# Kernel tuning notes

Hardware: AMD Instinct MI355X
Metric: run time of the kernel (lower is better)

## Reference

```python
import jax, jax.numpy as jnp
import numpy as np

D_IN = 1024
D_OUT = 1024
NUM_HEAD = 16
HEAD_DIM = D_OUT // NUM_HEAD
CTX = 2048


def setup_inputs() -> dict:
    key = jax.random.key(0)
    ks = jax.random.split(key, 7)
    s = 0.02
    x = jax.random.normal(ks[0], (2, CTX, D_IN), dtype=jnp.float32)
    Wq = jax.random.normal(ks[1], (D_IN, D_OUT), dtype=jnp.float32) * s
    Wk = jax.random.normal(ks[2], (D_IN, D_OUT), dtype=jnp.float32) * s
    Wv = jax.random.normal(ks[3], (D_IN, D_OUT), dtype=jnp.float32) * s
    Wo = jax.random.normal(ks[4], (D_OUT, D_OUT), dtype=jnp.float32) * s
    bo = jax.random.normal(ks[5], (D_OUT,), dtype=jnp.float32) * s
    return {"x": x, "Wq": Wq, "Wk": Wk, "Wv": Wv, "Wo": Wo, "bo": bo}


def reference(x, Wq, Wk, Wv, Wo, bo):
    B, T, _ = x.shape
    # QKV projections, split into heads: [B, H, T, hd]
    def split_heads(y):
        return y.reshape(B, T, NUM_HEAD, HEAD_DIM).transpose(0, 2, 1, 3)
    q = split_heads(x @ Wq)
    k = split_heads(x @ Wk)
    v = split_heads(x @ Wv)
    # scaled causal attention scores [B, H, T, T]
    scores = jnp.einsum("bhqd,bhkd->bhqk", q, k) / jnp.sqrt(
        jnp.asarray(HEAD_DIM, dtype=x.dtype))
    causal = jnp.tril(jnp.ones((T, T), dtype=bool))  # mask buffer triu(diag=1) -> keep lower tri
    scores = jnp.where(causal[None, None], scores, jnp.asarray(-jnp.inf, dtype=x.dtype))
    attn = jax.nn.softmax(scores, axis=-1)
    # dropout with droprate=0.0 is identity
    ctx = jnp.einsum("bhqk,bhkd->bhqd", attn, v)
    ctx = ctx.transpose(0, 2, 1, 3).reshape(B, T, D_OUT)
    return ctx @ Wo + bo
```

## Files before the change

### kernel.cpp

```cpp
#include <hip/hip_runtime.h>

typedef __bf16 bf16x8 __attribute__((ext_vector_type(8)));
typedef float f32x4 __attribute__((ext_vector_type(4)));
typedef float f32x16 __attribute__((ext_vector_type(16)));
typedef unsigned int u32x4 __attribute__((ext_vector_type(4)));

__device__ inline unsigned short f2bf(float f) {
    unsigned int x = __builtin_bit_cast(unsigned int, f);
    x += 0x7fff + ((x >> 16) & 1);
    return (unsigned short)(x >> 16);
}

__device__ __forceinline__ void gl_lds16(const unsigned short* g, unsigned short* l)
{
    __builtin_amdgcn_global_load_lds(
        (const __attribute__((address_space(1))) void*)g,
        (__attribute__((address_space(3))) void*)l, 16, 0, 0);
}

__global__ __launch_bounds__(256)
void prep(const float* __restrict__ x, unsigned short* __restrict__ xb,
          const float* __restrict__ Wq, const float* __restrict__ Wk,
          const float* __restrict__ Wv, unsigned short* __restrict__ wT)
{
    __shared__ unsigned short T[64][72];
    if (blockIdx.x < 2048) {
        const size_t i = ((size_t)blockIdx.x * 256 + threadIdx.x) * 8;
        float4 a = *reinterpret_cast<const float4*>(x + i);
        float4 b = *reinterpret_cast<const float4*>(x + i + 4);
        unsigned short t[8] = { f2bf(a.x), f2bf(a.y), f2bf(a.z), f2bf(a.w),
                                f2bf(b.x), f2bf(b.y), f2bf(b.z), f2bf(b.w) };
        *reinterpret_cast<uint4*>(xb + i) = *reinterpret_cast<uint4*>(t);
        return;
    }
    const int blk = blockIdx.x - 2048;
    const int z = blk >> 8, within = blk & 255;
    const float* W = (z == 0) ? Wq : (z == 1) ? Wk : Wv;
    unsigned short* dstBase = wT + (size_t)z * 1024 * 1024;
    const int k0 = (within >> 4) * 64, n0 = (within & 15) * 64;
    const int r = threadIdx.x >> 2, c0 = (threadIdx.x & 3) * 16;
    const float* src = W + (size_t)(k0 + r) * 1024 + n0 + c0;
    #pragma unroll
    for (int j = 0; j < 16; j += 4) {
        float4 f = *reinterpret_cast<const float4*>(src + j);
        T[r][c0 + j]     = f2bf(f.x);
        T[r][c0 + j + 1] = f2bf(f.y);
        T[r][c0 + j + 2] = f2bf(f.z);
        T[r][c0 + j + 3] = f2bf(f.w);
    }
    __syncthreads();
    unsigned short* dst = dstBase + (size_t)(n0 + r) * 1024 + k0 + c0;
    #pragma unroll
    for (int h = 0; h < 2; ++h) {
        unsigned short t8[8];
        #pragma unroll
        for (int j = 0; j < 8; ++j) t8[j] = T[c0 + h * 8 + j][r];
        *reinterpret_cast<uint4*>(dst + h * 8) = *reinterpret_cast<uint4*>(t8);
    }
}

__global__ __launch_bounds__(256)
void wconv(const float* __restrict__ W, unsigned short* __restrict__ wT)
{
    __shared__ unsigned short T[64][72];
    const int k0 = blockIdx.y * 64, n0 = blockIdx.x * 64;
    const int r = threadIdx.x >> 2, c0 = (threadIdx.x & 3) * 16;
    const float* src = W + (size_t)(k0 + r) * 1024 + n0 + c0;
    #pragma unroll
    for (int j = 0; j < 16; j += 4) {
        float4 f = *reinterpret_cast<const float4*>(src + j);
        T[r][c0 + j]     = f2bf(f.x);
        T[r][c0 + j + 1] = f2bf(f.y);
        T[r][c0 + j + 2] = f2bf(f.z);
        T[r][c0 + j + 3] = f2bf(f.w);
    }
    __syncthreads();
    unsigned short* dst = wT + (size_t)(n0 + r) * 1024 + k0 + c0;
    #pragma unroll
    for (int h = 0; h < 2; ++h) {
        unsigned short t8[8];
        #pragma unroll
        for (int j = 0; j < 8; ++j) t8[j] = T[c0 + h * 8 + j][r];
        *reinterpret_cast<uint4*>(dst + h * 8) = *reinterpret_cast<uint4*>(t8);
    }
}

__global__ __launch_bounds__(512, 4)
void gemm8p(const unsigned short* __restrict__ A,
            const unsigned short* __restrict__ BT,
            unsigned short* __restrict__ qb,
            unsigned short* __restrict__ kb,
            unsigned short* __restrict__ vT)
{
    __shared__ unsigned short As[2][128 * 64];
    __shared__ unsigned short Bs[2][192 * 64];

    const int tid  = threadIdx.x;
    const int wave = tid >> 6, lane = tid & 63;
    const int quad = lane >> 4, l16 = lane & 15;
    const int wm = wave >> 2, wn = wave & 3;
    const int mBase = blockIdx.y * 128, nBase = blockIdx.x * 192;

    f32x4 acc[4][3] = {};

    const int arow = tid >> 3;
    const int u8   = (tid & 7) ^ (arow & 7);
    const int rx   = l16 & 7;

    auto stage = [&](int kb0, int buf) {
        #pragma unroll
        for (int i = 0; i < 2; ++i)
            gl_lds16(A + (size_t)(mBase + i * 64 + arow) * 1024 + kb0 + u8 * 8,
                     &As[buf][(i * 512 + wave * 64) * 8]);
        #pragma unroll
        for (int i = 0; i < 3; ++i)
            gl_lds16(BT + (size_t)(nBase + i * 64 + arow) * 1024 + kb0 + u8 * 8,
                     &Bs[buf][(i * 512 + wave * 64) * 8]);
    };

    stage(0, 0);
    __syncthreads();

    for (int t = 0; t < 16; ++t) {
        const int buf = t & 1;
        if (t + 1 < 16)
            stage((t + 1) * 64, buf ^ 1);

        #pragma unroll
        for (int kh = 0; kh < 2; ++kh) {
            bf16x8 af[4], bf[3];
            #pragma unroll
            for (int mr = 0; mr < 4; ++mr) {
                const int row = wm * 64 + mr * 16 + l16;
                af[mr] = *reinterpret_cast<const bf16x8*>(
                    &As[buf][row * 64 + (((kh * 4 + quad) ^ rx) * 8)]);
            }
            #pragma unroll
            for (int nr = 0; nr < 3; ++nr) {
                const int row = wn * 48 + nr * 16 + l16;
                bf[nr] = *reinterpret_cast<const bf16x8*>(
                    &Bs[buf][row * 64 + (((kh * 4 + quad) ^ rx) * 8)]);
            }
            #pragma unroll
            for (int mr = 0; mr < 4; ++mr)
                #pragma unroll
                for (int nr = 0; nr < 3; ++nr)
                    acc[mr][nr] = __builtin_amdgcn_mfma_f32_16x16x32_bf16(
                        af[mr], bf[nr], acc[mr][nr], 0, 0, 0);
        }

        if (t + 1 < 16) {
            asm volatile("s_waitcnt vmcnt(0)" ::: "memory");
            __builtin_amdgcn_s_barrier();
        }
    }

    #pragma unroll
    for (int mr = 0; mr < 4; ++mr) {
        const int row0 = mBase + wm * 64 + mr * 16 + quad * 4;
        #pragma unroll
        for (int nr = 0; nr < 3; ++nr) {
            const int col = nBase + wn * 48 + nr * 16 + l16;
            if (col < 1024) {
                #pragma unroll
                for (int i = 0; i < 4; ++i)
                    qb[(size_t)(row0 + i) * 1024 + col] = f2bf(acc[mr][nr][i]);
            } else if (col < 2048) {
                #pragma unroll
                for (int i = 0; i < 4; ++i)
                    kb[(size_t)(row0 + i) * 1024 + col - 1024] = f2bf(acc[mr][nr][i]);
            } else {
                unsigned short t4[4] = { f2bf(acc[mr][nr][0]), f2bf(acc[mr][nr][1]),
                                         f2bf(acc[mr][nr][2]), f2bf(acc[mr][nr][3]) };
                *reinterpret_cast<uint2*>(&vT[(size_t)(col - 2048) * 4096 + row0]) =
                    *reinterpret_cast<uint2*>(t4);
            }
        }
    }
}

__global__ __launch_bounds__(256)
void gemm128o(const unsigned short* __restrict__ A,
              const unsigned short* __restrict__ BT,
              float* __restrict__ out, const float* __restrict__ bias)
{
    __shared__ unsigned short As[128 * 32];
    __shared__ unsigned short Bs[128 * 32];

    const int tid = threadIdx.x;
    const int wave = tid >> 6, lane = tid & 63, quad = lane >> 4, l16 = lane & 15;
    const int wm = wave >> 1, wn = wave & 1;
    const int mBase = blockIdx.y * 128, nBase = blockIdx.x * 128;

    f32x4 acc[4][4] = {};

    const int srow = lane >> 2, sko = (lane & 3) * 8;

    for (int kb = 0; kb < 1024; kb += 32) {
        __syncthreads();
        #pragma unroll
        for (int j = 0; j < 2; ++j) {
            const int seg = wave * 2 + j;
            gl_lds16(A  + (size_t)(mBase + seg * 16 + srow) * 1024 + kb + sko,
                     As + seg * 512);
            gl_lds16(BT + (size_t)(nBase + seg * 16 + srow) * 1024 + kb + sko,
                     Bs + seg * 512);
        }
        __syncthreads();

        bf16x8 af[4], bf[4];
        #pragma unroll
        for (int t = 0; t < 4; ++t) {
            af[t] = *reinterpret_cast<const bf16x8*>(&As[(wm * 64 + t * 16 + l16) * 32 + quad * 8]);
            bf[t] = *reinterpret_cast<const bf16x8*>(&Bs[(wn * 64 + t * 16 + l16) * 32 + quad * 8]);
        }
        #pragma unroll
        for (int ti = 0; ti < 4; ++ti)
            #pragma unroll
            for (int tj = 0; tj < 4; ++tj)
                acc[ti][tj] = __builtin_amdgcn_mfma_f32_16x16x32_bf16(
                    af[ti], bf[tj], acc[ti][tj], 0, 0, 0);
    }

    #pragma unroll
    for (int ti = 0; ti < 4; ++ti) {
        const int row0 = mBase + wm * 64 + ti * 16 + quad * 4;
        #pragma unroll
        for (int tj = 0; tj < 4; ++tj) {
            const int col = nBase + wn * 64 + tj * 16 + l16;
            const float ba = bias[col];
            #pragma unroll
            for (int i = 0; i < 4; ++i)
                out[(size_t)(row0 + i) * 1024 + col] = acc[ti][tj][i] + ba;
        }
    }
}

__global__ __launch_bounds__(256, 2)
void attn12(const unsigned short* __restrict__ q,
            const unsigned short* __restrict__ k,
            const unsigned short* __restrict__ vT,
            unsigned short* __restrict__ ctx)
{
    __shared__ unsigned short Ks[3][64 * 64];
    __shared__ unsigned short Vs[3][64 * 64];
    __shared__ float Lt[8 * 64];

    const int tid  = threadIdx.x;
    const int wave = tid >> 6, lane = tid & 63;
    const int q32 = lane & 31, hi = lane >> 5;
    const int slice = wave & 1;
    const int ks    = wave >> 1;
    const int L   = (int)(blockIdx.x + (blockIdx.y << 4));
    const int xcd = L & 7, idx = L >> 3;
    const int bh  = xcd * 4 + (idx >> 4);
    const int j   = idx & 15;
    const int b = bh >> 4, h = bh & 15;
    const int tokBase = b * 2048;
    const int colBase = h * 64;
    const int qtA = 31 - j, qtB = j;
    const int qloA = qtA * 64 + slice * 32;
    const int qloB = qtB * 64 + slice * 32;

    bf16x8 aqA[4], aqB[4];
    {
        const unsigned short* ra = q + (size_t)(tokBase + qloA + q32) * 1024 + colBase + hi * 8;
        const unsigned short* rb = q + (size_t)(tokBase + qloB + q32) * 1024 + colBase + hi * 8;
        #pragma unroll
        for (int c = 0; c < 4; ++c) {
            aqA[c] = *reinterpret_cast<const bf16x8*>(ra + c * 16);
            aqB[c] = *reinterpret_cast<const bf16x8*>(rb + c * 16);
        }
    }
    #pragma unroll
    for (int c = 0; c < 4; ++c)
        asm volatile("" :: "v"(aqA[c]), "v"(aqB[c]));

    f32x16 oA[2] = {}, oB[2] = {};
    float lsA = 0.0f, lsB = 0.0f;

    const int s0 = (wave * 2 + 0) * 64 + lane;
    const int s1 = (wave * 2 + 1) * 64 + lane;
    const int r0 = s0 >> 3, sw0 = (s0 & 7) ^ (r0 & 7);
    const int r1 = s1 >> 3, sw1 = (s1 & 7) ^ (r1 & 7);
    const size_t kOff0 = (size_t)r0 * 1024 + colBase + sw0 * 8;
    const size_t kOff1 = (size_t)r1 * 1024 + colBase + sw1 * 8;
    const size_t vOff0 = (size_t)(colBase + r0) * 4096 + sw0 * 8;
    const size_t vOff1 = (size_t)(colBase + r1) * 4096 + sw1 * 8;

    auto stage = [&](int tok0, int buf) {
        gl_lds16(k  + (size_t)tok0 * 1024 + kOff0, &Ks[buf][(wave * 2 + 0) * 512]);
        gl_lds16(k  + (size_t)tok0 * 1024 + kOff1, &Ks[buf][(wave * 2 + 1) * 512]);
        gl_lds16(vT + vOff0 + tok0,                &Vs[buf][(wave * 2 + 0) * 512]);
        gl_lds16(vT + vOff1 + tok0,                &Vs[buf][(wave * 2 + 1) * 512]);
    };

    bf16x8 ak[4];
    bf16x8 bv[2][2];

    const int nkt = qtA + 1;
    stage(tokBase, 0);
    stage(tokBase + 64, 1);

    int cur = 0;
    const int krowK = ks * 32 + q32;
    for (int kt = 0; kt < nkt; ++kt) {
        if (kt + 1 < nkt) asm volatile("s_waitcnt vmcnt(4)" ::: "memory");
        else              asm volatile("s_waitcnt vmcnt(0)" ::: "memory");
        __builtin_amdgcn_s_barrier();
        asm volatile("" ::: "memory");

        const int stg = (cur == 0) ? 2 : cur - 1;
        if (kt + 2 < nkt)
            stage(tokBase + (kt + 2) * 64, stg);

        const unsigned short* KsB = Ks[cur];
        const unsigned short* VsB = Vs[cur];
        #pragma unroll
        for (int c = 0; c < 4; ++c) {
            const int u = c * 2 + hi;
            ak[c] = *reinterpret_cast<const bf16x8*>(
                &KsB[krowK * 64 + ((u ^ (krowK & 7)) * 8)]);
        }
        #pragma unroll
        for (int kc = 0; kc < 2; ++kc)
            #pragma unroll
            for (int dh = 0; dh < 2; ++dh) {
                const int vrow = dh * 32 + q32;
                const int u = ks * 4 + kc * 2 + hi;
                bv[kc][dh] = *reinterpret_cast<const bf16x8*>(
                    &VsB[vrow * 64 + ((u ^ (vrow & 7)) * 8)]);
            }

        const int klo = kt * 64 + ks * 32;
        const bool dB = (klo <= qloB + 31);
        const bool dA = (klo <= qloA + 31);

        if (dB) {
            f32x16 scA = (f32x16)0.0f, scB = (f32x16)0.0f;
            #pragma unroll
            for (int c = 0; c < 4; ++c) {
                scA = __builtin_amdgcn_mfma_f32_32x32x16_bf16(ak[c], aqA[c], scA, 0, 0, 0);
                scB = __builtin_amdgcn_mfma_f32_32x32x16_bf16(ak[c], aqB[c], scB, 0, 0, 0);
            }
            float pA[16], pB[16];
            #pragma unroll
            for (int r = 0; r < 16; ++r) {
                pA[r] = __expf(scA[r] * 0.125f);
                pB[r] = __expf(scB[r] * 0.125f);
            }
            if (klo + 31 > qloB) {
                #pragma unroll
                for (int r = 0; r < 16; ++r) {
                    const int krow = (r & 3) + 8 * (r >> 2) + 4 * hi;
                    if (klo + krow > qloB + q32) pB[r] = 0.0f;
                }
            }
            #pragma unroll
            for (int r = 0; r < 16; ++r) { lsA += pA[r]; lsB += pB[r]; }
            unsigned int pkA[8], pkB[8];
            #pragma unroll
            for (int i = 0; i < 8; ++i) {
                asm("v_cvt_pk_bf16_f32 %0, %1, %2"
                    : "=v"(pkA[i]) : "v"(pA[2 * i]), "v"(pA[2 * i + 1]));
                asm("v_cvt_pk_bf16_f32 %0, %1, %2"
                    : "=v"(pkB[i]) : "v"(pB[2 * i]), "v"(pB[2 * i + 1]));
            }
            #pragma unroll
            for (int kc = 0; kc < 2; ++kc) {
                unsigned int xa0 = pkA[kc * 4 + 0], ya0 = pkA[kc * 4 + 2];
                unsigned int xa1 = pkA[kc * 4 + 1], ya1 = pkA[kc * 4 + 3];
                unsigned int xb0 = pkB[kc * 4 + 0], yb0 = pkB[kc * 4 + 2];
                unsigned int xb1 = pkB[kc * 4 + 1], yb1 = pkB[kc * 4 + 3];
                asm("v_permlane32_swap_b32 %0, %1" : "+v"(xa0), "+v"(ya0));
                asm("v_permlane32_swap_b32 %0, %1" : "+v"(xa1), "+v"(ya1));
                asm("v_permlane32_swap_b32 %0, %1" : "+v"(xb0), "+v"(yb0));
                asm("v_permlane32_swap_b32 %0, %1" : "+v"(xb1), "+v"(yb1));
                const u32x4 wa = { xa0, xa1, ya0, ya1 };
                const u32x4 wb = { xb0, xb1, yb0, yb1 };
                const bf16x8 paA = __builtin_bit_cast(bf16x8, wa);
                const bf16x8 paB = __builtin_bit_cast(bf16x8, wb);
                #pragma unroll
                for (int dh = 0; dh < 2; ++dh) {
                    oA[dh] = __builtin_amdgcn_mfma_f32_32x32x16_bf16(paA, bv[kc][dh], oA[dh], 0, 0, 0);
                    oB[dh] = __builtin_amdgcn_mfma_f32_32x32x16_bf16(paB, bv[kc][dh], oB[dh], 0, 0, 0);
                }
            }
        } else if (dA) {
            f32x16 sc = (f32x16)0.0f;
            #pragma unroll
            for (int c = 0; c < 4; ++c)
                sc = __builtin_amdgcn_mfma_f32_32x32x16_bf16(ak[c], aqA[c], sc, 0, 0, 0);
            float p[16];
            #pragma unroll
            for (int r = 0; r < 16; ++r) p[r] = __expf(sc[r] * 0.125f);
            if (klo + 31 > qloA) {
                #pragma unroll
                for (int r = 0; r < 16; ++r) {
                    const int krow = (r & 3) + 8 * (r >> 2) + 4 * hi;
                    if (klo + krow > qloA + q32) p[r] = 0.0f;
                }
            }
            #pragma unroll
            for (int r = 0; r < 16; ++r) lsA += p[r];
            unsigned int pk[8];
            #pragma unroll
            for (int i = 0; i < 8; ++i)
                asm("v_cvt_pk_bf16_f32 %0, %1, %2"
                    : "=v"(pk[i]) : "v"(p[2 * i]), "v"(p[2 * i + 1]));
            #pragma unroll
            for (int kc = 0; kc < 2; ++kc) {
                unsigned int x0 = pk[kc * 4 + 0], y0 = pk[kc * 4 + 2];
                unsigned int x1 = pk[kc * 4 + 1], y1 = pk[kc * 4 + 3];
                asm("v_permlane32_swap_b32 %0, %1" : "+v"(x0), "+v"(y0));
                asm("v_permlane32_swap_b32 %0, %1" : "+v"(x1), "+v"(y1));
                const u32x4 wv = { x0, x1, y0, y1 };
                const bf16x8 pa = __builtin_bit_cast(bf16x8, wv);
                #pragma unroll
                for (int dh = 0; dh < 2; ++dh)
                    oA[dh] = __builtin_amdgcn_mfma_f32_32x32x16_bf16(pa, bv[kc][dh], oA[dh], 0, 0, 0);
            }
        }
        cur = (cur == 2) ? 0 : cur + 1;
    }

    float* Obuf = reinterpret_cast<float*>(&Ks[0][0]);

    __syncthreads();
    Lt[(wave * 2 + 0) * 64 + lane] = lsA;
    Lt[(wave * 2 + 1) * 64 + lane] = lsB;

    auto writePartial = [&](const f32x16 (&o)[2]) {
        float* slot = Obuf + slice * 2048;
        #pragma unroll
        for (int r = 0; r < 16; ++r) {
            const int row = (r & 3) + 8 * (r >> 2) + 4 * hi;
            #pragma unroll
            for (int dh = 0; dh < 2; ++dh)
                slot[row * 64 + dh * 32 + q32] = o[dh][r];
        }
    };
    auto finalize = [&](int t, int qt, const f32x16 (&o)[2]) {
        const float lf = Lt[(slice * 2 + t) * 64 + q32]
                       + Lt[(slice * 2 + t) * 64 + 32 + q32]
                       + Lt[((slice + 2) * 2 + t) * 64 + q32]
                       + Lt[((slice + 2) * 2 + t) * 64 + 32 + q32];
        const float inv = 1.0f / lf;
        const float* slot = Obuf + slice * 2048;
        #pragma unroll
        for (int r = 0; r < 16; ++r) {
            const int row = (r & 3) + 8 * (r >> 2) + 4 * hi;
            const float invr = __shfl(inv, row);
            const size_t gr = (size_t)(tokBase + qt * 64 + slice * 32 + row) * 1024 + colBase;
            #pragma unroll
            for (int dh = 0; dh < 2; ++dh)
                ctx[gr + dh * 32 + q32] =
                    f2bf((o[dh][r] + slot[row * 64 + dh * 32 + q32]) * invr);
        }
    };

    if (ks == 1) writePartial(oA);
    __syncthreads();
    if (ks == 0) finalize(0, qtA, oA);
    __syncthreads();
    if (ks == 0) writePartial(oB);
    __syncthreads();
    if (ks == 1) finalize(1, qtB, oB);
}

extern "C" void kernel_launch(void* const* d_in, const int* in_sizes, int n_in,
                              void* d_out, int out_size, void* d_ws, size_t ws_size,
                              hipStream_t stream)
{
    const float* x  = (const float*)d_in[0];
    const float* Wq = (const float*)d_in[1];
    const float* Wk = (const float*)d_in[2];
    const float* Wv = (const float*)d_in[3];
    const float* Wo = (const float*)d_in[4];
    const float* bo = (const float*)d_in[5];
    float* out = (float*)d_out;

    unsigned short* xb     = (unsigned short*)d_ws;
    unsigned short* qb     = xb + (size_t)4096 * 1024;
    unsigned short* kb     = qb + (size_t)4096 * 1024;
    unsigned short* vT     = kb + (size_t)4096 * 1024;
    unsigned short* ctx    = xb;
    unsigned short* wqkvT  = (unsigned short*)d_out;
    unsigned short* woT    = kb;

    prep<<<2816, 256, 0, stream>>>(x, xb, Wq, Wk, Wv, wqkvT);

    gemm8p<<<dim3(16, 32), 512, 0, stream>>>(xb, wqkvT, qb, kb, vT);

    attn12<<<dim3(16, 32), 256, 0, stream>>>(qb, kb, vT, ctx);

    wconv<<<dim3(16, 16), 256, 0, stream>>>(Wo, woT);

    gemm128o<<<dim3(8, 32), 256, 0, stream>>>(ctx, woT, out, bo);
}
```

Measured before the change: 175.8 us.

## Rewrite output projection GEMM with double-buffered swizzled LDS and 128x64 tiles

Replaces the output-projection GEMM with a version that double-buffers LDS tiles so the next K-slab load overlaps with MFMA work, uses a larger K step of 64, and XOR-swizzles LDS layout to avoid bank conflicts. The tile shrinks to 128x64 so the grid grows from 256 to 512 blocks, which is meant to fill more CUs, with launch bounds allowing two blocks per CU. This costs more LDS per block and a larger share of redundant A loads.

```diff
diff --git a/kernel.cpp b/kernel.cpp
--- a/kernel.cpp
+++ b/kernel.cpp
@@ -179,59 +179,84 @@
     }
 }
 
-__global__ __launch_bounds__(256)
-void gemm128o(const unsigned short* __restrict__ A,
-              const unsigned short* __restrict__ BT,
-              float* __restrict__ out, const float* __restrict__ bias)
-{
-    __shared__ unsigned short As[128 * 32];
-    __shared__ unsigned short Bs[128 * 32];
-
-    const int tid = threadIdx.x;
-    const int wave = tid >> 6, lane = tid & 63, quad = lane >> 4, l16 = lane & 15;
+__global__ __launch_bounds__(256, 2)
+void gemm_op(const unsigned short* __restrict__ A,
+             const unsigned short* __restrict__ BT,
+             float* __restrict__ out, const float* __restrict__ bias)
+{
+    __shared__ unsigned short As[2][128 * 64];
+    __shared__ unsigned short Bs[2][64 * 64];
+
+    const int tid  = threadIdx.x;
+    const int wave = tid >> 6, lane = tid & 63;
+    const int quad = lane >> 4, l16 = lane & 15;
     const int wm = wave >> 1, wn = wave & 1;
-    const int mBase = blockIdx.y * 128, nBase = blockIdx.x * 128;
-
-    f32x4 acc[4][4] = {};
-
-    const int srow = lane >> 2, sko = (lane & 3) * 8;
-
-    for (int kb = 0; kb < 1024; kb += 32) {
-        __syncthreads();
-        #pragma unroll
-        for (int j = 0; j < 2; ++j) {
-            const int seg = wave * 2 + j;
-            gl_lds16(A  + (size_t)(mBase + seg * 16 + srow) * 1024 + kb + sko,
-                     As + seg * 512);
-            gl_lds16(BT + (size_t)(nBase + seg * 16 + srow) * 1024 + kb + sko,
-                     Bs + seg * 512);
-        }
-        __syncthreads();
-
-        bf16x8 af[4], bf[4];
-        #pragma unroll
-        for (int t = 0; t < 4; ++t) {
-            af[t] = *reinterpret_cast<const bf16x8*>(&As[(wm * 64 + t * 16 + l16) * 32 + quad * 8]);
-            bf[t] = *reinterpret_cast<const bf16x8*>(&Bs[(wn * 64 + t * 16 + l16) * 32 + quad * 8]);
-        }
-        #pragma unroll
-        for (int ti = 0; ti < 4; ++ti)
-            #pragma unroll
-            for (int tj = 0; tj < 4; ++tj)
-                acc[ti][tj] = __builtin_amdgcn_mfma_f32_16x16x32_bf16(
-                    af[ti], bf[tj], acc[ti][tj], 0, 0, 0);
-    }
-
-    #pragma unroll
-    for (int ti = 0; ti < 4; ++ti) {
-        const int row0 = mBase + wm * 64 + ti * 16 + quad * 4;
-        #pragma unroll
-        for (int tj = 0; tj < 4; ++tj) {
-            const int col = nBase + wn * 64 + tj * 16 + l16;
+    const int mBase = blockIdx.y * 128, nBase = blockIdx.x * 64;
+
+    f32x4 acc[4][2] = {};
+
+    const int arow = tid >> 3;
+    const int u8   = (tid & 7) ^ (arow & 7);
+    const int rx   = l16 & 7;
+
+    auto stage = [&](int kb0, int buf) {
+        #pragma unroll
+        for (int i = 0; i < 4; ++i)
+            gl_lds16(A + (size_t)(mBase + i * 32 + arow) * 1024 + kb0 + u8 * 8,
+                     &As[buf][(i * 256 + tid) * 8]);
+        #pragma unroll
+        for (int i = 0; i < 2; ++i)
+            gl_lds16(BT + (size_t)(nBase + i * 32 + arow) * 1024 + kb0 + u8 * 8,
+                     &Bs[buf][(i * 256 + tid) * 8]);
+    };
+
+    stage(0, 0);
+    __syncthreads();
+
+    for (int t = 0; t < 16; ++t) {
+        const int buf = t & 1;
+        if (t + 1 < 16)
+            stage((t + 1) * 64, buf ^ 1);
+
+        #pragma unroll
+        for (int kh = 0; kh < 2; ++kh) {
+            bf16x8 af[4], bf[2];
+            #pragma unroll
+            for (int mr = 0; mr < 4; ++mr) {
+                const int row = wm * 64 + mr * 16 + l16;
+                af[mr] = *reinterpret_cast<const bf16x8*>(
+                    &As[buf][row * 64 + (((kh * 4 + quad) ^ rx) * 8)]);
+            }
+            #pragma unroll
+            for (int nr = 0; nr < 2; ++nr) {
+                const int row = wn * 32 + nr * 16 + l16;
+                bf[nr] = *reinterpret_cast<const bf16x8*>(
+                    &Bs[buf][row * 64 + (((kh * 4 + quad) ^ rx) * 8)]);
+            }
+            #pragma unroll
+            for (int mr = 0; mr < 4; ++mr)
+                #pragma unroll
+                for (int nr = 0; nr < 2; ++nr)
+                    acc[mr][nr] = __builtin_amdgcn_mfma_f32_16x16x32_bf16(
+                        af[mr], bf[nr], acc[mr][nr], 0, 0, 0);
+        }
+
+        if (t + 1 < 16) {
+            asm volatile("s_waitcnt vmcnt(0)" ::: "memory");
+            __builtin_amdgcn_s_barrier();
+        }
+    }
+
+    #pragma unroll
+    for (int mr = 0; mr < 4; ++mr) {
+        const int row0 = mBase + wm * 64 + mr * 16 + quad * 4;
+        #pragma unroll
+        for (int nr = 0; nr < 2; ++nr) {
+            const int col = nBase + wn * 32 + nr * 16 + l16;
             const float ba = bias[col];
             #pragma unroll
             for (int i = 0; i < 4; ++i)
-                out[(size_t)(row0 + i) * 1024 + col] = acc[ti][tj][i] + ba;
+                out[(size_t)(row0 + i) * 1024 + col] = acc[mr][nr][i] + ba;
         }
     }
 }
@@ -496,5 +521,5 @@
 
     wconv<<<dim3(16, 16), 256, 0, stream>>>(Wo, woT);
 
-    gemm128o<<<dim3(8, 32), 256, 0, stream>>>(ctx, woT, out, bo);
-}
+    gemm_op<<<dim3(16, 32), 256, 0, stream>>>(ctx, woT, out, bo);
+}
```

Measured after the change: 175.1 us. About the same (-0.4%).
